# Optimization experiments

Hardware: AMD Instinct MI355X
Metric: run time of the kernel (lower is better)

## Reference

```python
import jax, jax.numpy as jnp
import numpy as np

NUM_CLASS = 20
ALPHA = 1.0
BETA = 1.0
IGNORE = 255


def _fdiff(f, ax):
    """np.gradient/torch.gradient with unit spacing along axis ax (edge_order=1)."""
    n = f.shape[ax]
    sl = lambda a, b: jax.lax.slice_in_dim(f, a, b, axis=ax)
    interior = (sl(2, n) - sl(0, n - 2)) * 0.5
    first = sl(1, 2) - sl(0, 1)
    last = sl(n - 1, n) - sl(n - 2, n - 1)
    return jnp.concatenate([first, interior, last], axis=ax)


def _lga(targets):
    # one-hot over all classes at once: [C, B, D, H, W]
    cls = jnp.arange(NUM_CLASS, dtype=targets.dtype)[:, None, None, None, None]
    oh = (targets[None] == cls).astype(jnp.float32)
    res = jnp.zeros(targets.shape, jnp.float32)
    for ax in (2, 3, 4):  # spatial dims of [C,B,D,H,W]
        res = res + jnp.sum(jnp.abs(_fdiff(oh, ax)), axis=0)
    return res  # [B, D, H, W]


def setup_inputs() -> dict:
    key = jax.random.key(0)
    k1, k2, k3, k4 = jax.random.split(key, 4)
    B, D, H, W = 1, 256, 256, 32
    predictions = jax.random.normal(k1, (B, NUM_CLASS, D, H, W), dtype=jnp.float32)
    targets = jax.random.randint(k2, (B, D, H, W), 0, NUM_CLASS)
    ignore = jax.random.uniform(k3, (B, D, H, W)) < 0.02
    targets = jnp.where(ignore, IGNORE, targets).astype(jnp.int32)
    class_weights = jax.random.uniform(k4, (NUM_CLASS,), dtype=jnp.float32) + 0.1
    return {"predictions": predictions, "targets": targets, "class_weights": class_weights}


def reference(predictions, targets, class_weights):
    targets = targets.astype(jnp.int32)
    valid = targets != IGNORE
    t = jnp.where(valid, targets, 0)
    # weighted CE, reduction='none': -w[t] * log_softmax(pred)[t], 0 at ignore
    logp = jax.nn.log_softmax(predictions, axis=1)
    logp_t = jnp.take_along_axis(logp, t[:, None], axis=1)[:, 0]  # [B,D,H,W]
    w = class_weights[t]
    loss = jnp.where(valid, -w * logp_t, 0.0)
    lga_weights = ALPHA + BETA * _lga(targets)
    num = jnp.sum(loss * lga_weights)
    den = jnp.sum(jnp.where(valid, w, 0.0))
    return num / den
```

## Files before the change

### kernel.cpp

```cpp
#include <hip/hip_runtime.h>

#define NUM_CLASS 20
#define IGNORE_V 255
#define WW 32
#define HH 256
#define DDEPTH 256
#define NVOX (DDEPTH * HH * WW)

__device__ __forceinline__ float fpair(int a, int b) {
    if (a == b) return 0.0f;
    return (a == IGNORE_V || b == IGNORE_V) ? 1.0f : 2.0f;
}

__global__ void pal_init(float* acc) {
    acc[0] = 0.0f;
    acc[1] = 0.0f;
}

__global__ __launch_bounds__(256) void pal_main(
    const float* __restrict__ pred,
    const int*   __restrict__ tgt,
    const float* __restrict__ cw,
    float*       __restrict__ acc)
{
    const int gid = blockIdx.x * blockDim.x + threadIdx.x;
    const int v0  = gid * 4;

    int4 t4 = *reinterpret_cast<const int4*>(tgt + v0);
    int t[4] = {t4.x, t4.y, t4.z, t4.w};

    float m[4], s[4], pt[4];
    {
        float4 x = *reinterpret_cast<const float4*>(pred + v0);
        float xx[4] = {x.x, x.y, x.z, x.w};
        #pragma unroll
        for (int j = 0; j < 4; j++) {
            m[j] = xx[j];
            s[j] = 1.0f;
            pt[j] = (t[j] == 0) ? xx[j] : 0.0f;
        }
    }
    #pragma unroll
    for (int c = 1; c < NUM_CLASS; c++) {
        float4 x = *reinterpret_cast<const float4*>(pred + (size_t)c * NVOX + v0);
        float xx[4] = {x.x, x.y, x.z, x.w};
        #pragma unroll
        for (int j = 0; j < 4; j++) {
            float nm = fmaxf(m[j], xx[j]);
            s[j] = s[j] * __expf(m[j] - nm) + __expf(xx[j] - nm);
            m[j] = nm;
            if (t[j] == c) pt[j] = xx[j];
        }
    }

    float num = 0.0f, den = 0.0f;
    #pragma unroll
    for (int j = 0; j < 4; j++) {
        const int v = v0 + j;
        const int w = v & (WW - 1);
        const int h = (v >> 5) & (HH - 1);
        const int d = v >> 13;
        float lga = 0.0f;
        {
            int im = v - ((w == 0) ? 0 : 1);
            int ip = v + ((w == WW - 1) ? 0 : 1);
            float sc = (w == 0 || w == WW - 1) ? 1.0f : 0.5f;
            lga += sc * fpair(tgt[im], tgt[ip]);
        }
        {
            int im = v - ((h == 0) ? 0 : WW);
            int ip = v + ((h == HH - 1) ? 0 : WW);
            float sc = (h == 0 || h == HH - 1) ? 1.0f : 0.5f;
            lga += sc * fpair(tgt[im], tgt[ip]);
        }
        {
            int im = v - ((d == 0) ? 0 : WW * HH);
            int ip = v + ((d == DDEPTH - 1) ? 0 : WW * HH);
            float sc = (d == 0 || d == DDEPTH - 1) ? 1.0f : 0.5f;
            lga += sc * fpair(tgt[im], tgt[ip]);
        }
        const int tj = t[j];
        if (tj != IGNORE_V) {
            float wt  = cw[tj];
            float lse = m[j] + __logf(s[j]);
            num += wt * (lse - pt[j]) * (1.0f + lga);
            den += wt;
        }
    }

    #pragma unroll
    for (int off = 32; off > 0; off >>= 1) {
        num += __shfl_down(num, off);
        den += __shfl_down(den, off);
    }
    __shared__ float sn[4], sd[4];
    const int lane = threadIdx.x & 63;
    const int wid  = threadIdx.x >> 6;
    if (lane == 0) { sn[wid] = num; sd[wid] = den; }
    __syncthreads();
    if (threadIdx.x == 0) {
        float n = sn[0] + sn[1] + sn[2] + sn[3];
        float d2 = sd[0] + sd[1] + sd[2] + sd[3];
        atomicAdd(&acc[0], n);
        atomicAdd(&acc[1], d2);
    }
}

__global__ void pal_final(const float* acc, float* out) {
    out[0] = acc[0] / acc[1];
}

extern "C" void kernel_launch(void* const* d_in, const int* in_sizes, int n_in,
                              void* d_out, int out_size, void* d_ws, size_t ws_size,
                              hipStream_t stream) {
    const float* pred = (const float*)d_in[0];
    const int*   tgt  = (const int*)d_in[1];
    const float* cw   = (const float*)d_in[2];
    float* out = (float*)d_out;
    float* acc = (float*)d_ws;

    pal_init<<<1, 1, 0, stream>>>(acc);
    const int threads = 256;
    const int blocks  = (NVOX / 4) / threads;
    pal_main<<<blocks, threads, 0, stream>>>(pred, tgt, cw, acc);
    pal_final<<<1, 1, 0, stream>>>(acc, out);
}
```

Baseline: 258.3 us.

## Split classes across lane quads, drop max-subtract, fuse final divide into main kernel

After: 607.2 us. 2.35x slower.

```diff
diff --git a/kernel.cpp b/kernel.cpp
--- a/kernel.cpp
+++ b/kernel.cpp
@@ -8,84 +8,93 @@
 #define NVOX (DDEPTH * HH * WW)
 
 __device__ __forceinline__ float fpair(int a, int b) {
-    if (a == b) return 0.0f;
-    return (a == IGNORE_V || b == IGNORE_V) ? 1.0f : 2.0f;
+    return (a == b) ? 0.0f : ((a == IGNORE_V || b == IGNORE_V) ? 1.0f : 2.0f);
 }
 
 __global__ void pal_init(float* acc) {
     acc[0] = 0.0f;
     acc[1] = 0.0f;
+    ((unsigned*)acc)[2] = 0u;
 }
 
-__global__ __launch_bounds__(256) void pal_main(
+__global__ __launch_bounds__(256, 8) void pal_main(
     const float* __restrict__ pred,
     const int*   __restrict__ tgt,
     const float* __restrict__ cw,
-    float*       __restrict__ acc)
+    float*       __restrict__ acc,
+    float*       __restrict__ out)
 {
+    __shared__ float lcw[NUM_CLASS];
+    if (threadIdx.x < NUM_CLASS) lcw[threadIdx.x] = cw[threadIdx.x];
+    __syncthreads();
+
     const int gid = blockIdx.x * blockDim.x + threadIdx.x;
-    const int v0  = gid * 4;
+    const int g   = gid & 3;
+    const int v0  = gid & ~3;
 
-    int4 t4 = *reinterpret_cast<const int4*>(tgt + v0);
-    int t[4] = {t4.x, t4.y, t4.z, t4.w};
+    const int4 t4 = *reinterpret_cast<const int4*>(tgt + v0);
+    const int t[4] = {t4.x, t4.y, t4.z, t4.w};
 
-    float m[4], s[4], pt[4];
-    {
-        float4 x = *reinterpret_cast<const float4*>(pred + v0);
-        float xx[4] = {x.x, x.y, x.z, x.w};
+    const float* p0 = pred + (size_t)(g * 5) * NVOX + v0;
+    float4 x[5];
+    #pragma unroll
+    for (int k = 0; k < 5; k++)
+        x[k] = *reinterpret_cast<const float4*>(p0 + (size_t)k * NVOX);
+
+    float s[4]  = {0.f, 0.f, 0.f, 0.f};
+    float pt[4] = {0.f, 0.f, 0.f, 0.f};
+    #pragma unroll
+    for (int k = 0; k < 5; k++) {
+        const int c = g * 5 + k;
+        const float xx[4] = {x[k].x, x[k].y, x[k].z, x[k].w};
         #pragma unroll
         for (int j = 0; j < 4; j++) {
-            m[j] = xx[j];
-            s[j] = 1.0f;
-            pt[j] = (t[j] == 0) ? xx[j] : 0.0f;
-        }
-    }
-    #pragma unroll
-    for (int c = 1; c < NUM_CLASS; c++) {
-        float4 x = *reinterpret_cast<const float4*>(pred + (size_t)c * NVOX + v0);
-        float xx[4] = {x.x, x.y, x.z, x.w};
-        #pragma unroll
-        for (int j = 0; j < 4; j++) {
-            float nm = fmaxf(m[j], xx[j]);
-            s[j] = s[j] * __expf(m[j] - nm) + __expf(xx[j] - nm);
-            m[j] = nm;
+            s[j] += __expf(xx[j]);
             if (t[j] == c) pt[j] = xx[j];
         }
     }
 
-    float num = 0.0f, den = 0.0f;
     #pragma unroll
     for (int j = 0; j < 4; j++) {
-        const int v = v0 + j;
+        s[j]  += __shfl_xor(s[j], 1);
+        s[j]  += __shfl_xor(s[j], 2);
+        pt[j] += __shfl_xor(pt[j], 1);
+        pt[j] += __shfl_xor(pt[j], 2);
+    }
+
+    const int v  = v0 + g;
+    const float sg  = (g == 0) ? s[0]  : (g == 1) ? s[1]  : (g == 2) ? s[2]  : s[3];
+    const float ptg = (g == 0) ? pt[0] : (g == 1) ? pt[1] : (g == 2) ? pt[2] : pt[3];
+    const int   tj  = (g == 0) ? t[0]  : (g == 1) ? t[1]  : (g == 2) ? t[2]  : t[3];
+
+    float num = 0.0f, den = 0.0f;
+    if (tj != IGNORE_V) {
         const int w = v & (WW - 1);
         const int h = (v >> 5) & (HH - 1);
         const int d = v >> 13;
-        float lga = 0.0f;
+        float lga;
         {
-            int im = v - ((w == 0) ? 0 : 1);
-            int ip = v + ((w == WW - 1) ? 0 : 1);
-            float sc = (w == 0 || w == WW - 1) ? 1.0f : 0.5f;
-            lga += sc * fpair(tgt[im], tgt[ip]);
+            const int tL = tgt[v - ((w != 0)      ? 1 : 0)];
+            const int tR = tgt[v + ((w != WW - 1) ? 1 : 0)];
+            const float sc = (w == 0 || w == WW - 1) ? 1.0f : 0.5f;
+            lga = sc * fpair(tL, tR);
         }
         {
-            int im = v - ((h == 0) ? 0 : WW);
-            int ip = v + ((h == HH - 1) ? 0 : WW);
-            float sc = (h == 0 || h == HH - 1) ? 1.0f : 0.5f;
-            lga += sc * fpair(tgt[im], tgt[ip]);
+            const int tU = tgt[v - ((h != 0)      ? WW : 0)];
+            const int tD = tgt[v + ((h != HH - 1) ? WW : 0)];
+            const float sc = (h == 0 || h == HH - 1) ? 1.0f : 0.5f;
+            lga += sc * fpair(tU, tD);
         }
         {
-            int im = v - ((d == 0) ? 0 : WW * HH);
-            int ip = v + ((d == DDEPTH - 1) ? 0 : WW * HH);
-            float sc = (d == 0 || d == DDEPTH - 1) ? 1.0f : 0.5f;
-            lga += sc * fpair(tgt[im], tgt[ip]);
+            const int tB = tgt[v - ((d != 0)          ? WW * HH : 0)];
+            const int tF = tgt[v + ((d != DDEPTH - 1) ? WW * HH : 0)];
+            const float sc = (d == 0 || d == DDEPTH - 1) ? 1.0f : 0.5f;
+            lga += sc * fpair(tB, tF);
         }
-        const int tj = t[j];
-        if (tj != IGNORE_V) {
-            float wt  = cw[tj];
-            float lse = m[j] + __logf(s[j]);
-            num += wt * (lse - pt[j]) * (1.0f + lga);
-            den += wt;
-        }
+        const float wt  = lcw[tj];
+        const float lse = __logf(sg);
+        num = wt * (lse - ptg) * (1.0f + lga);
+        den = wt;
     }
 
     #pragma unroll
@@ -99,15 +108,18 @@
     if (lane == 0) { sn[wid] = num; sd[wid] = den; }
     __syncthreads();
     if (threadIdx.x == 0) {
-        float n = sn[0] + sn[1] + sn[2] + sn[3];
-        float d2 = sd[0] + sd[1] + sd[2] + sd[3];
+        const float n  = sn[0] + sn[1] + sn[2] + sn[3];
+        const float d2 = sd[0] + sd[1] + sd[2] + sd[3];
         atomicAdd(&acc[0], n);
         atomicAdd(&acc[1], d2);
+        __threadfence();
+        const unsigned ticket = atomicAdd((unsigned*)&acc[2], 1u);
+        if (ticket == gridDim.x - 1) {
+            const float fn = atomicAdd(&acc[0], 0.0f);
+            const float fd = atomicAdd(&acc[1], 0.0f);
+            out[0] = fn / fd;
+        }
     }
-}
-
-__global__ void pal_final(const float* acc, float* out) {
-    out[0] = acc[0] / acc[1];
 }
 
 extern "C" void kernel_launch(void* const* d_in, const int* in_sizes, int n_in,
@@ -121,7 +133,6 @@
 
     pal_init<<<1, 1, 0, stream>>>(acc);
     const int threads = 256;
-    const int blocks  = (NVOX / 4) / threads;
-    pal_main<<<blocks, threads, 0, stream>>>(pred, tgt, cw, acc);
-    pal_final<<<1, 1, 0, stream>>>(acc, out);
+    const int blocks  = NVOX / threads;
+    pal_main<<<blocks, threads, 0, stream>>>(pred, tgt, cw, acc, out);
 }
```

## Process one voxel per thread with batched logit loads and max-free softmax

Applied to the files above, without the earlier changes.

Result: slower. 394.9 us (+52.9%).

```diff
diff --git a/kernel.cpp b/kernel.cpp
--- a/kernel.cpp
+++ b/kernel.cpp
@@ -8,8 +8,7 @@
 #define NVOX (DDEPTH * HH * WW)
 
 __device__ __forceinline__ float fpair(int a, int b) {
-    if (a == b) return 0.0f;
-    return (a == IGNORE_V || b == IGNORE_V) ? 1.0f : 2.0f;
+    return (a == b) ? 0.0f : ((a == IGNORE_V || b == IGNORE_V) ? 1.0f : 2.0f);
 }
 
 __global__ void pal_init(float* acc) {
@@ -23,69 +22,54 @@
     const float* __restrict__ cw,
     float*       __restrict__ acc)
 {
-    const int gid = blockIdx.x * blockDim.x + threadIdx.x;
-    const int v0  = gid * 4;
+    __shared__ float lcw[NUM_CLASS];
+    if (threadIdx.x < NUM_CLASS) lcw[threadIdx.x] = cw[threadIdx.x];
+    __syncthreads();
 
-    int4 t4 = *reinterpret_cast<const int4*>(tgt + v0);
-    int t[4] = {t4.x, t4.y, t4.z, t4.w};
+    const int v = blockIdx.x * blockDim.x + threadIdx.x;
+    const int w = v & (WW - 1);
+    const int h = (v >> 5) & (HH - 1);
+    const int d = v >> 13;
 
-    float m[4], s[4], pt[4];
-    {
-        float4 x = *reinterpret_cast<const float4*>(pred + v0);
-        float xx[4] = {x.x, x.y, x.z, x.w};
-        #pragma unroll
-        for (int j = 0; j < 4; j++) {
-            m[j] = xx[j];
-            s[j] = 1.0f;
-            pt[j] = (t[j] == 0) ? xx[j] : 0.0f;
-        }
+    const int t  = tgt[v];
+    const int tL = tgt[v - ((w != 0)          ? 1       : 0)];
+    const int tR = tgt[v + ((w != WW - 1)     ? 1       : 0)];
+    const int tU = tgt[v - ((h != 0)          ? WW      : 0)];
+    const int tD = tgt[v + ((h != HH - 1)     ? WW      : 0)];
+    const int tB = tgt[v - ((d != 0)          ? WW * HH : 0)];
+    const int tF = tgt[v + ((d != DDEPTH - 1) ? WW * HH : 0)];
+
+    float x[NUM_CLASS];
+    #pragma unroll
+    for (int c = 0; c < NUM_CLASS; c++)
+        x[c] = pred[(size_t)c * NVOX + v];
+
+    float s0 = 0.f, s1 = 0.f, s2 = 0.f, s3 = 0.f;
+    float pt = 0.f;
+    #pragma unroll
+    for (int c = 0; c < NUM_CLASS; c += 4) {
+        s0 += __expf(x[c]);
+        s1 += __expf(x[c + 1]);
+        s2 += __expf(x[c + 2]);
+        s3 += __expf(x[c + 3]);
+        pt = (t == c)     ? x[c]     : pt;
+        pt = (t == c + 1) ? x[c + 1] : pt;
+        pt = (t == c + 2) ? x[c + 2] : pt;
+        pt = (t == c + 3) ? x[c + 3] : pt;
     }
-    #pragma unroll
-    for (int c = 1; c < NUM_CLASS; c++) {
-        float4 x = *reinterpret_cast<const float4*>(pred + (size_t)c * NVOX + v0);
-        float xx[4] = {x.x, x.y, x.z, x.w};
-        #pragma unroll
-        for (int j = 0; j < 4; j++) {
-            float nm = fmaxf(m[j], xx[j]);
-            s[j] = s[j] * __expf(m[j] - nm) + __expf(xx[j] - nm);
-            m[j] = nm;
-            if (t[j] == c) pt[j] = xx[j];
-        }
-    }
+    const float s = (s0 + s1) + (s2 + s3);
 
     float num = 0.0f, den = 0.0f;
-    #pragma unroll
-    for (int j = 0; j < 4; j++) {
-        const int v = v0 + j;
-        const int w = v & (WW - 1);
-        const int h = (v >> 5) & (HH - 1);
-        const int d = v >> 13;
-        float lga = 0.0f;
-        {
-            int im = v - ((w == 0) ? 0 : 1);
-            int ip = v + ((w == WW - 1) ? 0 : 1);
-            float sc = (w == 0 || w == WW - 1) ? 1.0f : 0.5f;
-            lga += sc * fpair(tgt[im], tgt[ip]);
-        }
-        {
-            int im = v - ((h == 0) ? 0 : WW);
-            int ip = v + ((h == HH - 1) ? 0 : WW);
-            float sc = (h == 0 || h == HH - 1) ? 1.0f : 0.5f;
-            lga += sc * fpair(tgt[im], tgt[ip]);
-        }
-        {
-            int im = v - ((d == 0) ? 0 : WW * HH);
-            int ip = v + ((d == DDEPTH - 1) ? 0 : WW * HH);
-            float sc = (d == 0 || d == DDEPTH - 1) ? 1.0f : 0.5f;
-            lga += sc * fpair(tgt[im], tgt[ip]);
-        }
-        const int tj = t[j];
-        if (tj != IGNORE_V) {
-            float wt  = cw[tj];
-            float lse = m[j] + __logf(s[j]);
-            num += wt * (lse - pt[j]) * (1.0f + lga);
-            den += wt;
-        }
+    if (t != IGNORE_V) {
+        const float scW = (w == 0 || w == WW - 1)     ? 1.0f : 0.5f;
+        const float scH = (h == 0 || h == HH - 1)     ? 1.0f : 0.5f;
+        const float scD = (d == 0 || d == DDEPTH - 1) ? 1.0f : 0.5f;
+        const float lga = scW * fpair(tL, tR)
+                        + scH * fpair(tU, tD)
+                        + scD * fpair(tB, tF);
+        const float wt = lcw[t];
+        num = wt * (__logf(s) - pt) * (1.0f + lga);
+        den = wt;
     }
 
     #pragma unroll
@@ -99,10 +83,8 @@
     if (lane == 0) { sn[wid] = num; sd[wid] = den; }
     __syncthreads();
     if (threadIdx.x == 0) {
-        float n = sn[0] + sn[1] + sn[2] + sn[3];
-        float d2 = sd[0] + sd[1] + sd[2] + sd[3];
-        atomicAdd(&acc[0], n);
-        atomicAdd(&acc[1], d2);
+        atomicAdd(&acc[0], (sn[0] + sn[1]) + (sn[2] + sn[3]));
+        atomicAdd(&acc[1], (sd[0] + sd[1]) + (sd[2] + sd[3]));
     }
 }
 
@@ -121,7 +103,7 @@
 
     pal_init<<<1, 1, 0, stream>>>(acc);
     const int threads = 256;
-    const int blocks  = (NVOX / 4) / threads;
+    const int blocks  = NVOX / threads;
     pal_main<<<blocks, threads, 0, stream>>>(pred, tgt, cw, acc);
     pal_final<<<1, 1, 0, stream>>>(acc, out);
 }
```
